# Kernel tuning notes

Hardware: AMD Instinct MI355X
Metric: run time of the kernel (lower is better)

Reference implementation:

```python
import jax, jax.numpy as jnp
import numpy as np

HIDDEN = 1024
HEADS = 16
HEAD = HIDDEN // HEADS


def setup_inputs() -> dict:
    key = jax.random.key(0)
    ks = jax.random.split(key, 10)
    s = 1.0 / np.sqrt(HIDDEN)
    inp = {
        "x": jax.random.normal(ks[0], (2, 2048, HIDDEN), dtype=jnp.float32),
        "Wq": jax.random.uniform(ks[1], (HIDDEN, HIDDEN), jnp.float32, -s, s),
        "bq": jnp.zeros((HIDDEN,), jnp.float32),
        "Wk": jax.random.uniform(ks[2], (HIDDEN, HIDDEN), jnp.float32, -s, s),
        "bk": jnp.zeros((HIDDEN,), jnp.float32),
        "Wv": jax.random.uniform(ks[3], (HIDDEN, HIDDEN), jnp.float32, -s, s),
        "bv": jnp.zeros((HIDDEN,), jnp.float32),
        "Wo": jax.random.uniform(ks[4], (HIDDEN, HIDDEN), jnp.float32, -s, s),
        "bo": jnp.zeros((HIDDEN,), jnp.float32),
        "ln_g": jnp.ones((HIDDEN,), jnp.float32),
        "ln_b": jnp.zeros((HIDDEN,), jnp.float32),
    }
    return inp


def reference(x, Wq, bq, Wk, bk, Wv, bv, Wo, bo, ln_g, ln_b):
    B, S, H = x.shape
    # pre-LN (eps=1e-5 like torch LayerNorm)
    mu = jnp.mean(x, axis=-1, keepdims=True)
    var = jnp.mean(jnp.square(x - mu), axis=-1, keepdims=True)
    xn = (x - mu) * jax.lax.rsqrt(var + 1e-5) * ln_g + ln_b
    # QKV projections (torch Linear: x @ W.T + b) -> [B,S,heads,head]
    q = (xn @ Wq.T + bq).reshape(B, S, HEADS, HEAD)
    k = (xn @ Wk.T + bk).reshape(B, S, HEADS, HEAD)
    v = (xn @ Wv.T + bv).reshape(B, S, HEADS, HEAD)
    # scaled dot-product attention, naive full scores [B,heads,S,S]
    scores = jnp.einsum("bqhd,bkhd->bhqk", q, k) / jnp.sqrt(jnp.float32(HEAD))
    attn = jax.nn.softmax(scores, axis=-1)
    ctx = jnp.einsum("bhqk,bkhd->bqhd", attn, v).reshape(B, S, H)
    out = ctx @ Wo.T + bo
    return x + out  # dropout is identity in eval
```

## Files before the change

### kernel.cpp

```cpp
#include <hip/hip_runtime.h>
#include <hip/hip_bf16.h>
#include <stdint.h>

#define HID 1024
#define SEQ 2048
#define BATCH 2
#define NHEADS 16
#define HEADDIM 64
#define MROWS (BATCH*SEQ)

#define GAS __attribute__((address_space(1)))
#define LAS __attribute__((address_space(3)))

typedef __attribute__((ext_vector_type(8))) __bf16 bf16x8;
typedef __attribute__((ext_vector_type(4))) float f32x4;
typedef __attribute__((ext_vector_type(2))) uint32_t u32x2;

__device__ __forceinline__ ushort f2bf(float f) {
  union { float f; uint32_t u; } v; v.f = f;
  return (ushort)((v.u + 0x7FFFu + ((v.u >> 16) & 1u)) >> 16);
}

__device__ __forceinline__ void gl_lds16(const void* g, void* l) {
  __builtin_amdgcn_global_load_lds((const GAS void*)g, (LAS void*)l, 16, 0, 0);
}

__global__ __launch_bounds__(256) void k_cvt(const float* __restrict__ Wq,
                                             const float* __restrict__ Wk,
                                             const float* __restrict__ Wv,
                                             const float* __restrict__ Wo,
                                             ushort* __restrict__ dst) {
  int mat = blockIdx.y;
  const float* src = (mat == 0) ? Wq : (mat == 1) ? Wk : (mat == 2) ? Wv : Wo;
  int off = (blockIdx.x * 256 + threadIdx.x) * 4;
  float4 v = *(const float4*)(src + off);
  ushort4 o;
  o.x = f2bf(v.x); o.y = f2bf(v.y); o.z = f2bf(v.z); o.w = f2bf(v.w);
  *(ushort4*)(dst + (size_t)mat * (HID * HID) + off) = o;
}

__global__ __launch_bounds__(256) void k_ln(const float* __restrict__ x,
                                            const float* __restrict__ g,
                                            const float* __restrict__ b,
                                            ushort* __restrict__ xn) {
  int row = blockIdx.x;
  int t = threadIdx.x;
  const float* xr = x + (size_t)row * HID;
  float4 v = *(const float4*)(xr + t * 4);
  float s = v.x + v.y + v.z + v.w;
  float s2 = v.x * v.x + v.y * v.y + v.z * v.z + v.w * v.w;
  for (int m = 1; m < 64; m <<= 1) { s += __shfl_xor(s, m); s2 += __shfl_xor(s2, m); }
  __shared__ float ws[4], ws2[4];
  int wid = t >> 6;
  if ((t & 63) == 0) { ws[wid] = s; ws2[wid] = s2; }
  __syncthreads();
  s = ws[0] + ws[1] + ws[2] + ws[3];
  s2 = ws2[0] + ws2[1] + ws2[2] + ws2[3];
  float mu = s * (1.0f / HID);
  float var = s2 * (1.0f / HID) - mu * mu;
  float rstd = rsqrtf(var + 1e-5f);
  float4 gg = *(const float4*)(g + t * 4);
  float4 bb = *(const float4*)(b + t * 4);
  ushort4 o;
  o.x = f2bf((v.x - mu) * rstd * gg.x + bb.x);
  o.y = f2bf((v.y - mu) * rstd * gg.y + bb.y);
  o.z = f2bf((v.z - mu) * rstd * gg.z + bb.z);
  o.w = f2bf((v.w - mu) * rstd * gg.w + bb.w);
  *(ushort4*)(xn + (size_t)row * HID + t * 4) = o;
}

__global__ __launch_bounds__(256) void k_qkv(const ushort* __restrict__ xn,
                                             const ushort* __restrict__ wmat,
                                             const float* __restrict__ bq,
                                             const float* __restrict__ bk,
                                             const float* __restrict__ bv,
                                             ushort* __restrict__ qo,
                                             ushort* __restrict__ ko,
                                             ushort* __restrict__ vo) {
  __shared__ ushort As[128 * 32];
  __shared__ ushort Bs[128 * 32];
  int tid = threadIdx.x;
  int lane = tid & 63;
  int wv = tid >> 6;
  int quad = lane >> 4;
  int l16 = lane & 15;
  int m0 = blockIdx.x * 128;
  int ng = blockIdx.y * 128;
  int mat = ng >> 10;
  int nloc = ng & 1023;
  const ushort* wptr = wmat + (size_t)mat * (HID * HID) + (size_t)nloc * HID;
  const float* bias = (mat == 0) ? bq : (mat == 1) ? bk : bv;
  ushort* outp = (mat == 0) ? qo : (mat == 1) ? ko : vo;
  const float scl = (mat == 0) ? 0.18033688011112042f : 1.0f;

  int arow = tid >> 2;
  int acol = (tid & 3) * 8;
  int wm = (wv >> 1) * 64, wn = (wv & 1) * 64;

  f32x4 acc[4][4] = {};
  for (int k0 = 0; k0 < HID; k0 += 32) {
    __syncthreads();
    for (int t = 0; t < 2; t++) {
      gl_lds16(xn + (size_t)(m0 + t * 64 + arow) * HID + k0 + acol,
               As + t * 2048 + wv * 512);
      gl_lds16(wptr + (size_t)(t * 64 + arow) * HID + k0 + acol,
               Bs + t * 2048 + wv * 512);
    }
    __syncthreads();
    bf16x8 af[4], bfr[4];
    for (int i = 0; i < 4; i++)
      af[i] = *(const bf16x8*)&As[(wm + i * 16 + l16) * 32 + quad * 8];
    for (int n = 0; n < 4; n++)
      bfr[n] = *(const bf16x8*)&Bs[(wn + n * 16 + l16) * 32 + quad * 8];
    for (int i = 0; i < 4; i++)
      for (int n = 0; n < 4; n++)
        acc[i][n] = __builtin_amdgcn_mfma_f32_16x16x32_bf16(af[i], bfr[n], acc[i][n], 0, 0, 0);
  }
  float bv4[4];
  for (int n = 0; n < 4; n++) bv4[n] = bias[nloc + wn + n * 16 + l16];
  for (int i = 0; i < 4; i++) {
    int mrow = m0 + wm + i * 16 + quad * 4;
    for (int n = 0; n < 4; n++) {
      int col = nloc + wn + n * 16 + l16;
      int h = col >> 6, d = col & 63;
      for (int r = 0; r < 4; r++) {
        int m = mrow + r;
        int bidx = m >> 11, sidx = m & 2047;
        size_t dst;
        if (mat == 2)
          dst = (((size_t)(bidx * NHEADS + h) * HEADDIM) + d) * SEQ + sidx;
        else
          dst = (((size_t)(bidx * NHEADS + h) * SEQ) + sidx) * HEADDIM + d;
        outp[dst] = f2bf((acc[i][n][r] + bv4[n]) * scl);
      }
    }
  }
}

__global__ __launch_bounds__(256, 2) void k_attn(const ushort* __restrict__ Q,
                                                 const ushort* __restrict__ K,
                                                 const ushort* __restrict__ Vt,
                                                 ushort* __restrict__ ctx) {
  __shared__ ushort Ksm[2][64 * 64];
  __shared__ ushort Vsm[2][64 * 64];
  __shared__ ushort Psm[4][32 * 64];
  int tid = threadIdx.x, lane = tid & 63, wv = tid >> 6, quad = lane >> 4, l16 = lane & 15;
  int bh = blockIdx.y;
  int q0 = blockIdx.x * 128;
  const ushort* Qb = Q + ((size_t)bh * SEQ + q0 + wv * 32) * HEADDIM;
  const ushort* Kb = K + (size_t)bh * SEQ * HEADDIM;
  const ushort* Vb = Vt + (size_t)bh * HEADDIM * SEQ;
  ushort* Pw = Psm[wv];

  bf16x8 qf[2][2];
  for (int m = 0; m < 2; m++)
    for (int c = 0; c < 2; c++)
      qf[m][c] = *(const bf16x8*)(Qb + (size_t)(m * 16 + l16) * HEADDIM + c * 32 + quad * 8);

  bf16x8 ones;
  for (int j = 0; j < 8; j++) ones[j] = (__bf16)1.0f;

  int gsl = lane & 7;
  int rowA = wv * 8 + (lane >> 3);
  int rowB = 32 + wv * 8 + (lane >> 3);
  const ushort* kSrcA = Kb + rowA * HEADDIM + ((gsl ^ ((rowA >> 2) & 7)) * 8);
  const ushort* kSrcB = Kb + rowB * HEADDIM + ((gsl ^ ((rowB >> 2) & 7)) * 8);
  const ushort* vSrcA = Vb + (size_t)rowA * SEQ + ((gsl ^ (rowA & 7)) * 8);
  const ushort* vSrcB = Vb + (size_t)rowB * SEQ + ((gsl ^ (rowB & 7)) * 8);
  int ldsA = wv * 512;
  int ldsB = 2048 + wv * 512;

  f32x4 Oa[2][4] = {};
  f32x4 Os[2] = {};
  int fk = l16 & 7;

  gl_lds16(kSrcA, &Ksm[0][ldsA]);
  gl_lds16(kSrcB, &Ksm[0][ldsB]);
  gl_lds16(vSrcA, &Vsm[0][ldsA]);
  gl_lds16(vSrcB, &Vsm[0][ldsB]);
  __syncthreads();

  for (int kt = 0; kt < SEQ / 64; kt++) {
    int buf = kt & 1;
    if (kt + 1 < SEQ / 64) {
      int nb = buf ^ 1;
      size_t ko = (size_t)(kt + 1) * 64 * HEADDIM;
      size_t vo = (size_t)(kt + 1) * 64;
      gl_lds16(kSrcA + ko, &Ksm[nb][ldsA]);
      gl_lds16(kSrcB + ko, &Ksm[nb][ldsB]);
      gl_lds16(vSrcA + vo, &Vsm[nb][ldsA]);
      gl_lds16(vSrcB + vo, &Vsm[nb][ldsB]);
    }

    f32x4 sacc[2][4] = {};
    for (int nt = 0; nt < 4; nt++) {
      int krow = 4 * l16 + nt;
      for (int c = 0; c < 2; c++) {
        int kb = c * 4 + quad;
        bf16x8 kf = *(const bf16x8*)&Ksm[buf][krow * 64 + ((kb ^ fk) * 8)];
        sacc[0][nt] = __builtin_amdgcn_mfma_f32_16x16x32_bf16(qf[0][c], kf, sacc[0][nt], 0, 0, 0);
        sacc[1][nt] = __builtin_amdgcn_mfma_f32_16x16x32_bf16(qf[1][c], kf, sacc[1][nt], 0, 0, 0);
      }
    }

    for (int m = 0; m < 2; m++) {
      for (int r = 0; r < 4; r++) {
        union { float f; uint32_t u; } p0, p1, p2, p3;
        p0.f = __builtin_amdgcn_exp2f(fminf(sacc[m][0][r], 80.f));
        p1.f = __builtin_amdgcn_exp2f(fminf(sacc[m][1][r], 80.f));
        p2.f = __builtin_amdgcn_exp2f(fminf(sacc[m][2][r], 80.f));
        p3.f = __builtin_amdgcn_exp2f(fminf(sacc[m][3][r], 80.f));
        uint32_t pk01 = __builtin_amdgcn_perm(p1.u, p0.u, 0x07060302u);
        uint32_t pk23 = __builtin_amdgcn_perm(p3.u, p2.u, 0x07060302u);
        int row = m * 16 + quad * 4 + r;
        int idx = (row * 8 + ((l16 >> 1) ^ (row & 7))) * 8 + (l16 & 1) * 4;
        *(u32x2*)&Pw[idx] = (u32x2){pk01, pk23};
      }
    }

    for (int c = 0; c < 2; c++) {
      int kb = c * 4 + quad;
      bf16x8 pf0 = *(const bf16x8*)&Pw[(l16 * 8 + (kb ^ fk)) * 8];
      bf16x8 pf1 = *(const bf16x8*)&Pw[((16 + l16) * 8 + (kb ^ fk)) * 8];
      Os[0] = __builtin_amdgcn_mfma_f32_16x16x32_bf16(pf0, ones, Os[0], 0, 0, 0);
      Os[1] = __builtin_amdgcn_mfma_f32_16x16x32_bf16(pf1, ones, Os[1], 0, 0, 0);
      for (int nt = 0; nt < 4; nt++) {
        int d = nt * 16 + l16;
        bf16x8 vf = *(const bf16x8*)&Vsm[buf][d * 64 + ((kb ^ fk) * 8)];
        Oa[0][nt] = __builtin_amdgcn_mfma_f32_16x16x32_bf16(pf0, vf, Oa[0][nt], 0, 0, 0);
        Oa[1][nt] = __builtin_amdgcn_mfma_f32_16x16x32_bf16(pf1, vf, Oa[1][nt], 0, 0, 0);
      }
    }
    __syncthreads();
  }

  int bidx = bh >> 4, h = bh & 15;
  for (int m = 0; m < 2; m++) {
    for (int r = 0; r < 4; r++) {
      float inv = 1.0f / Os[m][r];
      int sidx = q0 + wv * 32 + m * 16 + quad * 4 + r;
      size_t base = ((size_t)(bidx * SEQ) + sidx) * HID + h * HEADDIM;
      for (int nt = 0; nt < 4; nt++)
        ctx[base + nt * 16 + l16] = f2bf(Oa[m][nt][r] * inv);
    }
  }
}

__global__ __launch_bounds__(256) void k_oproj(const ushort* __restrict__ ctx,
                                               const ushort* __restrict__ wmat,
                                               const float* __restrict__ bo,
                                               const float* __restrict__ x,
                                               float* __restrict__ out) {
  __shared__ ushort As[128 * 32];
  __shared__ ushort Bs[128 * 32];
  int tid = threadIdx.x;
  int lane = tid & 63;
  int wv = tid >> 6;
  int quad = lane >> 4;
  int l16 = lane & 15;
  int m0 = blockIdx.x * 128;
  int n0 = blockIdx.y * 128;
  const ushort* wptr = wmat + (size_t)3 * (HID * HID) + (size_t)n0 * HID;
  int arow = tid >> 2;
  int acol = (tid & 3) * 8;
  int wm = (wv >> 1) * 64, wn = (wv & 1) * 64;

  f32x4 acc[4][4] = {};
  for (int k0 = 0; k0 < HID; k0 += 32) {
    __syncthreads();
    for (int t = 0; t < 2; t++) {
      gl_lds16(ctx + (size_t)(m0 + t * 64 + arow) * HID + k0 + acol,
               As + t * 2048 + wv * 512);
      gl_lds16(wptr + (size_t)(t * 64 + arow) * HID + k0 + acol,
               Bs + t * 2048 + wv * 512);
    }
    __syncthreads();
    bf16x8 af[4], bfr[4];
    for (int i = 0; i < 4; i++)
      af[i] = *(const bf16x8*)&As[(wm + i * 16 + l16) * 32 + quad * 8];
    for (int n = 0; n < 4; n++)
      bfr[n] = *(const bf16x8*)&Bs[(wn + n * 16 + l16) * 32 + quad * 8];
    for (int i = 0; i < 4; i++)
      for (int n = 0; n < 4; n++)
        acc[i][n] = __builtin_amdgcn_mfma_f32_16x16x32_bf16(af[i], bfr[n], acc[i][n], 0, 0, 0);
  }
  float bv4[4];
  for (int n = 0; n < 4; n++) bv4[n] = bo[n0 + wn + n * 16 + l16];
  for (int i = 0; i < 4; i++) {
    int mrow = m0 + wm + i * 16 + quad * 4;
    for (int n = 0; n < 4; n++) {
      int col = n0 + wn + n * 16 + l16;
      for (int r = 0; r < 4; r++) {
        size_t idx = (size_t)(mrow + r) * HID + col;
        out[idx] = acc[i][n][r] + bv4[n] + x[idx];
      }
    }
  }
}

extern "C" void kernel_launch(void* const* d_in, const int* in_sizes, int n_in,
                              void* d_out, int out_size, void* d_ws, size_t ws_size,
                              hipStream_t stream) {
  const float* x    = (const float*)d_in[0];
  const float* Wq   = (const float*)d_in[1];
  const float* bq   = (const float*)d_in[2];
  const float* Wk   = (const float*)d_in[3];
  const float* bk   = (const float*)d_in[4];
  const float* Wv   = (const float*)d_in[5];
  const float* bv   = (const float*)d_in[6];
  const float* Wo   = (const float*)d_in[7];
  const float* bo   = (const float*)d_in[8];
  const float* ln_g = (const float*)d_in[9];
  const float* ln_b = (const float*)d_in[10];
  float* out = (float*)d_out;

  const size_t MB = 1024 * 1024;
  ushort* ws_w = (ushort*)d_ws;
  ushort* xn   = (ushort*)((char*)d_ws + 8 * MB);
  ushort* Qw   = (ushort*)((char*)d_ws + 16 * MB);
  ushort* Kw   = (ushort*)((char*)d_ws + 24 * MB);
  ushort* Vw   = (ushort*)((char*)d_ws + 32 * MB);
  ushort* Cw   = (ushort*)((char*)d_ws + 40 * MB);

  k_cvt<<<dim3(1024, 4), 256, 0, stream>>>(Wq, Wk, Wv, Wo, ws_w);
  k_ln<<<dim3(MROWS), 256, 0, stream>>>(x, ln_g, ln_b, xn);
  k_qkv<<<dim3(32, 24), 256, 0, stream>>>(xn, ws_w, bq, bk, bv, Qw, Kw, Vw);
  k_attn<<<dim3(SEQ / 128, BATCH * NHEADS), 256, 0, stream>>>(Qw, Kw, Vw, Cw);
  k_oproj<<<dim3(32, 8), 256, 0, stream>>>(Cw, ws_w, bo, x, out);
}
```

Before: 210.4 us.

## Halve attention query tile per wave to raise occupancy

Reduces each wave's query rows from 32 to 16, shrinking the block tile to 64 queries and doubling the attention grid. Launch bounds move to 4 blocks per SM, and the P scratch buffer and register accumulators shrink. The aim is more resident waves to hide latency, at the cost of half the K/V reuse per LDS load and twice the global K/V traffic.

```diff
diff --git a/kernel.cpp b/kernel.cpp
--- a/kernel.cpp
+++ b/kernel.cpp
@@ -137,25 +137,24 @@
   }
 }
 
-__global__ __launch_bounds__(256, 2) void k_attn(const ushort* __restrict__ Q,
+__global__ __launch_bounds__(256, 4) void k_attn(const ushort* __restrict__ Q,
                                                  const ushort* __restrict__ K,
                                                  const ushort* __restrict__ Vt,
                                                  ushort* __restrict__ ctx) {
   __shared__ ushort Ksm[2][64 * 64];
   __shared__ ushort Vsm[2][64 * 64];
-  __shared__ ushort Psm[4][32 * 64];
+  __shared__ ushort Psm[4][16 * 64];
   int tid = threadIdx.x, lane = tid & 63, wv = tid >> 6, quad = lane >> 4, l16 = lane & 15;
   int bh = blockIdx.y;
-  int q0 = blockIdx.x * 128;
-  const ushort* Qb = Q + ((size_t)bh * SEQ + q0 + wv * 32) * HEADDIM;
+  int q0 = blockIdx.x * 64;
+  const ushort* Qb = Q + ((size_t)bh * SEQ + q0 + wv * 16) * HEADDIM;
   const ushort* Kb = K + (size_t)bh * SEQ * HEADDIM;
   const ushort* Vb = Vt + (size_t)bh * HEADDIM * SEQ;
   ushort* Pw = Psm[wv];
 
-  bf16x8 qf[2][2];
-  for (int m = 0; m < 2; m++)
-    for (int c = 0; c < 2; c++)
-      qf[m][c] = *(const bf16x8*)(Qb + (size_t)(m * 16 + l16) * HEADDIM + c * 32 + quad * 8);
+  bf16x8 qf[2];
+  for (int c = 0; c < 2; c++)
+    qf[c] = *(const bf16x8*)(Qb + (size_t)l16 * HEADDIM + c * 32 + quad * 8);
 
   bf16x8 ones;
   for (int j = 0; j < 8; j++) ones[j] = (__bf16)1.0f;
@@ -170,8 +169,8 @@
   int ldsA = wv * 512;
   int ldsB = 2048 + wv * 512;
 
-  f32x4 Oa[2][4] = {};
-  f32x4 Os[2] = {};
+  f32x4 Oa[4] = {};
+  f32x4 Os = {};
   int fk = l16 & 7;
 
   gl_lds16(kSrcA, &Ksm[0][ldsA]);
@@ -192,57 +191,49 @@
       gl_lds16(vSrcB + vo, &Vsm[nb][ldsB]);
     }
 
-    f32x4 sacc[2][4] = {};
+    f32x4 sacc[4] = {};
     for (int nt = 0; nt < 4; nt++) {
       int krow = 4 * l16 + nt;
       for (int c = 0; c < 2; c++) {
         int kb = c * 4 + quad;
         bf16x8 kf = *(const bf16x8*)&Ksm[buf][krow * 64 + ((kb ^ fk) * 8)];
-        sacc[0][nt] = __builtin_amdgcn_mfma_f32_16x16x32_bf16(qf[0][c], kf, sacc[0][nt], 0, 0, 0);
-        sacc[1][nt] = __builtin_amdgcn_mfma_f32_16x16x32_bf16(qf[1][c], kf, sacc[1][nt], 0, 0, 0);
+        sacc[nt] = __builtin_amdgcn_mfma_f32_16x16x32_bf16(qf[c], kf, sacc[nt], 0, 0, 0);
       }
     }
 
-    for (int m = 0; m < 2; m++) {
-      for (int r = 0; r < 4; r++) {
-        union { float f; uint32_t u; } p0, p1, p2, p3;
-        p0.f = __builtin_amdgcn_exp2f(fminf(sacc[m][0][r], 80.f));
-        p1.f = __builtin_amdgcn_exp2f(fminf(sacc[m][1][r], 80.f));
-        p2.f = __builtin_amdgcn_exp2f(fminf(sacc[m][2][r], 80.f));
-        p3.f = __builtin_amdgcn_exp2f(fminf(sacc[m][3][r], 80.f));
-        uint32_t pk01 = __builtin_amdgcn_perm(p1.u, p0.u, 0x07060302u);
-        uint32_t pk23 = __builtin_amdgcn_perm(p3.u, p2.u, 0x07060302u);
-        int row = m * 16 + quad * 4 + r;
-        int idx = (row * 8 + ((l16 >> 1) ^ (row & 7))) * 8 + (l16 & 1) * 4;
-        *(u32x2*)&Pw[idx] = (u32x2){pk01, pk23};
-      }
+    for (int r = 0; r < 4; r++) {
+      union { float f; uint32_t u; } p0, p1, p2, p3;
+      p0.f = __builtin_amdgcn_exp2f(fminf(sacc[0][r], 80.f));
+      p1.f = __builtin_amdgcn_exp2f(fminf(sacc[1][r], 80.f));
+      p2.f = __builtin_amdgcn_exp2f(fminf(sacc[2][r], 80.f));
+      p3.f = __builtin_amdgcn_exp2f(fminf(sacc[3][r], 80.f));
+      uint32_t pk01 = __builtin_amdgcn_perm(p1.u, p0.u, 0x07060302u);
+      uint32_t pk23 = __builtin_amdgcn_perm(p3.u, p2.u, 0x07060302u);
+      int row = quad * 4 + r;
+      int idx = (row * 8 + ((l16 >> 1) ^ (row & 7))) * 8 + (l16 & 1) * 4;
+      *(u32x2*)&Pw[idx] = (u32x2){pk01, pk23};
     }
 
     for (int c = 0; c < 2; c++) {
       int kb = c * 4 + quad;
       bf16x8 pf0 = *(const bf16x8*)&Pw[(l16 * 8 + (kb ^ fk)) * 8];
-      bf16x8 pf1 = *(const bf16x8*)&Pw[((16 + l16) * 8 + (kb ^ fk)) * 8];
-      Os[0] = __builtin_amdgcn_mfma_f32_16x16x32_bf16(pf0, ones, Os[0], 0, 0, 0);
-      Os[1] = __builtin_amdgcn_mfma_f32_16x16x32_bf16(pf1, ones, Os[1], 0, 0, 0);
+      Os = __builtin_amdgcn_mfma_f32_16x16x32_bf16(pf0, ones, Os, 0, 0, 0);
       for (int nt = 0; nt < 4; nt++) {
         int d = nt * 16 + l16;
         bf16x8 vf = *(const bf16x8*)&Vsm[buf][d * 64 + ((kb ^ fk) * 8)];
-        Oa[0][nt] = __builtin_amdgcn_mfma_f32_16x16x32_bf16(pf0, vf, Oa[0][nt], 0, 0, 0);
-        Oa[1][nt] = __builtin_amdgcn_mfma_f32_16x16x32_bf16(pf1, vf, Oa[1][nt], 0, 0, 0);
+        Oa[nt] = __builtin_amdgcn_mfma_f32_16x16x32_bf16(pf0, vf, Oa[nt], 0, 0, 0);
       }
     }
     __syncthreads();
   }
 
   int bidx = bh >> 4, h = bh & 15;
-  for (int m = 0; m < 2; m++) {
-    for (int r = 0; r < 4; r++) {
-      float inv = 1.0f / Os[m][r];
-      int sidx = q0 + wv * 32 + m * 16 + quad * 4 + r;
-      size_t base = ((size_t)(bidx * SEQ) + sidx) * HID + h * HEADDIM;
-      for (int nt = 0; nt < 4; nt++)
-        ctx[base + nt * 16 + l16] = f2bf(Oa[m][nt][r] * inv);
-    }
+  for (int r = 0; r < 4; r++) {
+    float inv = 1.0f / Os[r];
+    int sidx = q0 + wv * 16 + quad * 4 + r;
+    size_t base = ((size_t)(bidx * SEQ) + sidx) * HID + h * HEADDIM;
+    for (int nt = 0; nt < 4; nt++)
+      ctx[base + nt * 16 + l16] = f2bf(Oa[nt][r] * inv);
   }
 }
 
@@ -325,6 +316,6 @@
   k_cvt<<<dim3(1024, 4), 256, 0, stream>>>(Wq, Wk, Wv, Wo, ws_w);
   k_ln<<<dim3(MROWS), 256, 0, stream>>>(x, ln_g, ln_b, xn);
   k_qkv<<<dim3(32, 24), 256, 0, stream>>>(xn, ws_w, bq, bk, bv, Qw, Kw, Vw);
-  k_attn<<<dim3(SEQ / 128, BATCH * NHEADS), 256, 0, stream>>>(Qw, Kw, Vw, Cw);
+  k_attn<<<dim3(SEQ / 64, BATCH * NHEADS), 256, 0, stream>>>(Qw, Kw, Vw, Cw);
   k_oproj<<<dim3(32, 8), 256, 0, stream>>>(Cw, ws_w, bo, x, out);
 }
```

Result: no change. 213.9 us (+1.7%).
